# Kernel tuning notes

Hardware: AMD Instinct MI355X
Metric: run time of the kernel (lower is better)

Reference implementation:

```python
import jax, jax.numpy as jnp
import numpy as np

TAU = 0.2  # world.kgc_temp
EPS = 1e-12  # F.normalize eps


def _l2_normalize(z):
    n = jnp.linalg.norm(z, axis=1, keepdims=True)
    return z / jnp.maximum(n, EPS)


def setup_inputs() -> dict:
    key = jax.random.key(0)
    k1, k2 = jax.random.split(key)
    N, D = 8192, 512
    z1 = jax.random.normal(k1, (N, D), dtype=jnp.float32)
    z2 = jax.random.normal(k2, (N, D), dtype=jnp.float32)
    return {"z1": z1, "z2": z2}


def _semi_loss(h1, h2):
    # h1, h2: [N, D] already L2-normalized
    refl_sim = jnp.exp(jnp.matmul(h1, h1.T) / TAU)      # [N, N]
    between_sim = jnp.exp(jnp.matmul(h1, h2.T) / TAU)   # [N, N]
    denom = refl_sim.sum(axis=1) + between_sim.sum(axis=1) - jnp.diag(refl_sim)
    return -jnp.log(jnp.diag(between_sim) / denom)      # [N]


def reference(z1, z2):
    h1 = _l2_normalize(z1)
    h2 = _l2_normalize(z2)
    l1 = _semi_loss(h1, h2)
    l2 = _semi_loss(h2, h1)
    return jnp.sum((l1 + l2) * 0.5)
```

## Files before the change

kernel.cpp:

```cpp
#include <hip/hip_runtime.h>
#include <hip/hip_bf16.h>
#include <math.h>
#include <stdint.h>

#define N_ROWS 8192
#define DIM 512
#define INV_TAU 5.0f
#define EXP5 148.41315910257660342f

typedef float f32x4 __attribute__((ext_vector_type(4)));
typedef long long i64;

union PairU {
  int4 v;
  struct { i64 lo, hi; } s;
};

__device__ __forceinline__ void gload_lds16(const void* g, void* l) {
  __builtin_amdgcn_global_load_lds(
      (__attribute__((address_space(1))) void*)(void*)g,
      (__attribute__((address_space(3))) void*)l,
      16, 0, 0);
}

__global__ __launch_bounds__(256) void normalize_kernel(
    const float* __restrict__ z1, const float* __restrict__ z2,
    uint8_t* __restrict__ h1p, uint8_t* __restrict__ h2p,
    float* __restrict__ dvec,
    float* __restrict__ r1, float* __restrict__ r2,
    float* __restrict__ brow, float* __restrict__ bcol,
    float* __restrict__ out) {
  __shared__ __align__(16) uint8_t L[16384];
  const int t = threadIdx.x;
  const int lr = t >> 4;
  const int kb = t & 15;
  const int row = blockIdx.x * 16 + lr;
  const float4* p1 = (const float4*)(z1 + (size_t)row * DIM + kb * 32);
  const float4* p2 = (const float4*)(z2 + (size_t)row * DIM + kb * 32);
  float4 a[8], b[8];
  float s1 = 0.f, s2 = 0.f, s3 = 0.f;
#pragma unroll
  for (int i = 0; i < 8; i++) {
    a[i] = p1[i]; b[i] = p2[i];
    s1 += a[i].x*a[i].x + a[i].y*a[i].y + a[i].z*a[i].z + a[i].w*a[i].w;
    s2 += b[i].x*b[i].x + b[i].y*b[i].y + b[i].z*b[i].z + b[i].w*b[i].w;
    s3 += a[i].x*b[i].x + a[i].y*b[i].y + a[i].z*b[i].z + a[i].w*b[i].w;
  }
  for (int m = 1; m <= 8; m <<= 1) {
    s1 += __shfl_xor(s1, m);
    s2 += __shfl_xor(s2, m);
    s3 += __shfl_xor(s3, m);
  }
  const float inv1 = 1.0f / fmaxf(sqrtf(s1), 1e-12f);
  const float inv2 = 1.0f / fmaxf(sqrtf(s2), 1e-12f);
  int w1[8], w2[8];
#pragma unroll
  for (int i = 0; i < 8; i++) {
    int w = __builtin_amdgcn_cvt_pk_fp8_f32(a[i].x*inv1, a[i].y*inv1, 0, false);
    w1[i] = __builtin_amdgcn_cvt_pk_fp8_f32(a[i].z*inv1, a[i].w*inv1, w, true);
    w = __builtin_amdgcn_cvt_pk_fp8_f32(b[i].x*inv2, b[i].y*inv2, 0, false);
    w2[i] = __builtin_amdgcn_cvt_pk_fp8_f32(b[i].z*inv2, b[i].w*inv2, w, true);
  }
  union { i64 q; int d[2]; } u;
  const int lbase = (kb >> 1) * 1024 + lr * 16 + (kb & 1) * 8;
#pragma unroll
  for (int q = 0; q < 4; q++) {
    u.d[0] = w1[q*2]; u.d[1] = w1[q*2+1];
    *(i64*)(L + lbase + q * 256) = u.q;
    u.d[0] = w2[q*2]; u.d[1] = w2[q*2+1];
    *(i64*)(L + 8192 + lbase + q * 256) = u.q;
  }
  if (kb == 0) dvec[row] = s3 * inv1 * inv2;
  if (t < 16) {
    const int i = blockIdx.x * 16 + t;
    r1[i] = 0.f; r2[i] = 0.f; brow[i] = 0.f; bcol[i] = 0.f;
    if (i == 0) out[0] = 0.f;
  }
  __syncthreads();
  const size_t gb = (size_t)blockIdx.x * 8192;
  int4* g1 = (int4*)(h1p + gb);
  int4* g2 = (int4*)(h2p + gb);
  const int4* Lv = (const int4*)L;
  g1[t]       = Lv[t];
  g1[t + 256] = Lv[t + 256];
  g2[t]       = Lv[t + 512];
  g2[t + 256] = Lv[t + 768];
}

__global__ __launch_bounds__(512, 4) void expsum_kernel(
    const uint8_t* __restrict__ h1p, const uint8_t* __restrict__ h2p,
    float* __restrict__ r1, float* __restrict__ r2,
    float* __restrict__ brow, float* __restrict__ bcol) {
  __shared__ __align__(16) uint8_t Bs[65536];

  const int u = (blockIdx.x & 7) * 520 + (blockIdx.x >> 3);
  int bi = (int)((129.0 - sqrt(129.0 * 129.0 - 4.0 * (double)u)) * 0.5);
  while (bi * (129 - bi) > u) bi--;
  while ((bi + 1) * (128 - bi) <= u) bi++;
  const int bj = 2 * bi + (u - bi * (129 - bi));
  const bool needPred = (bj == 2 * bi) || (bj == 2 * bi + 1);

  const uint8_t* Ap = (bi < 32) ? h1p : h2p;
  const uint8_t* Bp = (bj < 64) ? h1p : h2p;
  float* rowsOut = (bi < 32) ? ((bj < 64) ? r1 : brow) : r2;
  float* colsOut = (bj < 64) ? r1 : ((bi < 32) ? bcol : r2);
  const int iOutBase = (bi & 31) * 256;
  const int jOutBase = (bj & 63) * 128;
  const int giBase = bi * 256;
  const int gjBase = bj * 128;

  const int t = threadIdx.x;
  const int w = t >> 6;
  const int lane = t & 63;
  const int l16 = lane & 15;
  const int kq = lane >> 4;

  const uint8_t* Abase =
      Ap + ((size_t)((bi & 31) * 16 + w * 2)) * 8192 + (size_t)lane * 16 + 3584;
  const uint8_t* aSt0 = Abase;
  const uint8_t* aSt1 = Abase + 8192;

  PairU Ar[3][2];
#pragma unroll
  for (int p = 0; p < 2; p++) {
    const int ofs = p * 1024 - 3584;
    Ar[p][0].v = *(const int4*)(aSt0 + ofs);
    Ar[p][1].v = *(const int4*)(aSt1 + ofs);
  }

  {
    const uint8_t* Bgp = Bp + (size_t)(bj & 63) * 65536;
#pragma unroll
    for (int rnd = 0; rnd < 8; rnd++)
      gload_lds16(Bgp + rnd * 8192 + t * 16, Bs + rnd * 8192 + t * 16);
  }

  f32x4 acc[2][8];
#pragma unroll
  for (int a = 0; a < 2; a++)
#pragma unroll
    for (int b = 0; b < 8; b++)
#pragma unroll
      for (int r = 0; r < 4; r++) acc[a][b][r] = 0.0f;

  __syncthreads();

#pragma unroll
  for (int kbp = 0; kbp < 8; kbp++) {
    const int cur = kbp % 3;
    if (kbp < 6) {
      const int nxt = (kbp + 2) % 3;
      const int ofs = (kbp + 2) * 1024 - 3584;
      Ar[nxt][0].v = *(const int4*)(aSt0 + ofs);
      Ar[nxt][1].v = *(const int4*)(aSt1 + ofs);
    }
    PairU Bf[8];
#pragma unroll
    for (int f = 0; f < 8; f++)
      Bf[f].v = *(const int4*)(Bs + f * 8192 + kbp * 1024 + lane * 16);
#pragma unroll
    for (int fm = 0; fm < 2; fm++)
#pragma unroll
      for (int fn = 0; fn < 8; fn++)
        acc[fm][fn] = __builtin_amdgcn_mfma_f32_16x16x32_fp8_fp8(
            Ar[cur][fm].s.lo, Bf[fn].s.lo, acc[fm][fn], 0, 0, 0);
#pragma unroll
    for (int fm = 0; fm < 2; fm++)
#pragma unroll
      for (int fn = 0; fn < 8; fn++)
        acc[fm][fn] = __builtin_amdgcn_mfma_f32_16x16x32_fp8_fp8(
            Ar[cur][fm].s.hi, Bf[fn].s.hi, acc[fm][fn], 0, 0, 0);
  }

  float rowp[2][4];
  float colp[8];
#pragma unroll
  for (int fm = 0; fm < 2; fm++)
#pragma unroll
    for (int r = 0; r < 4; r++) rowp[fm][r] = 0.0f;
#pragma unroll
  for (int fn = 0; fn < 8; fn++) colp[fn] = 0.0f;

  if (!needPred) {
#pragma unroll
    for (int fm = 0; fm < 2; fm++)
#pragma unroll
      for (int fn = 0; fn < 8; fn++)
#pragma unroll
        for (int r = 0; r < 4; r++) {
          const float e = __expf(acc[fm][fn][r] * INV_TAU);
          rowp[fm][r] += e;
          colp[fn] += e;
        }
  } else {
#pragma unroll
    for (int fm = 0; fm < 2; fm++)
#pragma unroll
      for (int fn = 0; fn < 8; fn++)
#pragma unroll
        for (int r = 0; r < 4; r++) {
          const int gi = giBase + w * 32 + fm * 16 + kq * 4 + r;
          const int gj = gjBase + fn * 16 + l16;
          const float e = __expf(acc[fm][fn][r] * INV_TAU);
          rowp[fm][r] += (gi <= gj) ? e : 0.0f;
          colp[fn] += (gi < gj) ? e : 0.0f;
        }
  }

  __syncthreads();
  float* lds_col = (float*)Bs;
  float* lds_row = lds_col + 128;
  if (t < 128) lds_col[t] = 0.0f;
  __syncthreads();

#pragma unroll
  for (int fm = 0; fm < 2; fm++) {
#pragma unroll
    for (int r = 0; r < 4; r++) {
      float v = rowp[fm][r];
      v += __shfl_xor(v, 1);
      v += __shfl_xor(v, 2);
      v += __shfl_xor(v, 4);
      v += __shfl_xor(v, 8);
      if (l16 == 0) lds_row[w * 32 + fm * 16 + kq * 4 + r] = v;
    }
  }
#pragma unroll
  for (int fn = 0; fn < 8; fn++) {
    float v = colp[fn];
    v += __shfl_xor(v, 16);
    v += __shfl_xor(v, 32);
    if (kq == 0) atomicAdd(&lds_col[fn * 16 + l16], v);
  }
  __syncthreads();

  if (t < 256) atomicAdd(&rowsOut[iOutBase + t], lds_row[t]);
  else if (t < 384) atomicAdd(&colsOut[jOutBase + (t - 256)], lds_col[t - 256]);
}

__global__ __launch_bounds__(256) void finalize_kernel(
    const float* __restrict__ r1, const float* __restrict__ r2,
    const float* __restrict__ brow, const float* __restrict__ bcol,
    const float* __restrict__ dvec, float* __restrict__ out) {
  const int i = blockIdx.x * 256 + threadIdx.x;
  const float den1 = r1[i] + brow[i] - EXP5;
  const float den2 = r2[i] + bcol[i] - EXP5;
  float v = 0.5f * (logf(den1) + logf(den2)) - INV_TAU * dvec[i];
  for (int m = 32; m; m >>= 1) v += __shfl_xor(v, m);
  __shared__ float red[4];
  const int wave = threadIdx.x >> 6;
  if ((threadIdx.x & 63) == 0) red[wave] = v;
  __syncthreads();
  if (threadIdx.x == 0) atomicAdd(out, red[0] + red[1] + red[2] + red[3]);
}

extern "C" void kernel_launch(void* const* d_in, const int* in_sizes, int n_in,
                              void* d_out, int out_size, void* d_ws, size_t ws_size,
                              hipStream_t stream) {
  const float* z1 = (const float*)d_in[0];
  const float* z2 = (const float*)d_in[1];
  float* out = (float*)d_out;

  char* ws = (char*)d_ws;
  uint8_t* h1p = (uint8_t*)ws;
  uint8_t* h2p = (uint8_t*)(ws + (4u << 20));
  float* r1   = (float*)(ws + (8u << 20));
  float* r2   = r1 + N_ROWS;
  float* brow = r2 + N_ROWS;
  float* bcol = brow + N_ROWS;
  float* dvec = bcol + N_ROWS;

  normalize_kernel<<<N_ROWS / 16, 256, 0, stream>>>(
      z1, z2, h1p, h2p, dvec, r1, r2, brow, bcol, out);
  expsum_kernel<<<4160, 512, 0, stream>>>(h1p, h2p, r1, r2, brow, bcol);
  finalize_kernel<<<N_ROWS / 256, 256, 0, stream>>>(r1, r2, brow, bcol, dvec, out);
}
```

Measured before the change: 207.4 us.

## Switch expsum GEMM to 32x32x16 FP8 MFMA with matching packed layout

The exp-sum kernel now issues 32x32x16 FP8 MFMA instructions with 16-wide accumulators instead of 16x16x32 tiles. Each wave computes a 32x128 tile with fewer, larger MFMAs and fewer LDS B-fragment loads per K step. The normalize kernel is reworked to 32-row blocks of 512 threads so the packed FP8 layout matches the new operand fragments. The epilogue index mapping, the diagonal masking and the row/column reductions are rewritten for the 32x32 output layout. This risks layout or indexing mistakes and changes register pressure.

```diff
diff --git a/kernel.cpp b/kernel.cpp
--- a/kernel.cpp
+++ b/kernel.cpp
@@ -8,7 +8,7 @@
 #define INV_TAU 5.0f
 #define EXP5 148.41315910257660342f
 
-typedef float f32x4 __attribute__((ext_vector_type(4)));
+typedef float f32x16 __attribute__((ext_vector_type(16)));
 typedef long long i64;
 
 union PairU {
@@ -23,18 +23,18 @@
       16, 0, 0);
 }
 
-__global__ __launch_bounds__(256) void normalize_kernel(
+__global__ __launch_bounds__(512) void normalize_kernel(
     const float* __restrict__ z1, const float* __restrict__ z2,
     uint8_t* __restrict__ h1p, uint8_t* __restrict__ h2p,
     float* __restrict__ dvec,
     float* __restrict__ r1, float* __restrict__ r2,
     float* __restrict__ brow, float* __restrict__ bcol,
     float* __restrict__ out) {
-  __shared__ __align__(16) uint8_t L[16384];
+  __shared__ __align__(16) uint8_t L[32768];
   const int t = threadIdx.x;
   const int lr = t >> 4;
   const int kb = t & 15;
-  const int row = blockIdx.x * 16 + lr;
+  const int row = blockIdx.x * 32 + lr;
   const float4* p1 = (const float4*)(z1 + (size_t)row * DIM + kb * 32);
   const float4* p2 = (const float4*)(z2 + (size_t)row * DIM + kb * 32);
   float4 a[8], b[8];
@@ -56,35 +56,30 @@
   int w1[8], w2[8];
 #pragma unroll
   for (int i = 0; i < 8; i++) {
-    int w = __builtin_amdgcn_cvt_pk_fp8_f32(a[i].x*inv1, a[i].y*inv1, 0, false);
-    w1[i] = __builtin_amdgcn_cvt_pk_fp8_f32(a[i].z*inv1, a[i].w*inv1, w, true);
-    w = __builtin_amdgcn_cvt_pk_fp8_f32(b[i].x*inv2, b[i].y*inv2, 0, false);
-    w2[i] = __builtin_amdgcn_cvt_pk_fp8_f32(b[i].z*inv2, b[i].w*inv2, w, true);
-  }
-  union { i64 q; int d[2]; } u;
-  const int lbase = (kb >> 1) * 1024 + lr * 16 + (kb & 1) * 8;
-#pragma unroll
-  for (int q = 0; q < 4; q++) {
-    u.d[0] = w1[q*2]; u.d[1] = w1[q*2+1];
-    *(i64*)(L + lbase + q * 256) = u.q;
-    u.d[0] = w2[q*2]; u.d[1] = w2[q*2+1];
-    *(i64*)(L + 8192 + lbase + q * 256) = u.q;
-  }
+    int wv = __builtin_amdgcn_cvt_pk_fp8_f32(a[i].x*inv1, a[i].y*inv1, 0, false);
+    w1[i] = __builtin_amdgcn_cvt_pk_fp8_f32(a[i].z*inv1, a[i].w*inv1, wv, true);
+    wv = __builtin_amdgcn_cvt_pk_fp8_f32(b[i].x*inv2, b[i].y*inv2, 0, false);
+    w2[i] = __builtin_amdgcn_cvt_pk_fp8_f32(b[i].z*inv2, b[i].w*inv2, wv, true);
+  }
+  *(int4*)(L + kb * 1024 + lr * 16)          = make_int4(w1[0], w1[1], w1[4], w1[5]);
+  *(int4*)(L + kb * 1024 + (lr + 32) * 16)   = make_int4(w1[2], w1[3], w1[6], w1[7]);
+  *(int4*)(L + 16384 + kb * 1024 + lr * 16)        = make_int4(w2[0], w2[1], w2[4], w2[5]);
+  *(int4*)(L + 16384 + kb * 1024 + (lr + 32) * 16) = make_int4(w2[2], w2[3], w2[6], w2[7]);
   if (kb == 0) dvec[row] = s3 * inv1 * inv2;
-  if (t < 16) {
-    const int i = blockIdx.x * 16 + t;
+  if (t < 32) {
+    const int i = blockIdx.x * 32 + t;
     r1[i] = 0.f; r2[i] = 0.f; brow[i] = 0.f; bcol[i] = 0.f;
     if (i == 0) out[0] = 0.f;
   }
   __syncthreads();
-  const size_t gb = (size_t)blockIdx.x * 8192;
+  const size_t gb = (size_t)blockIdx.x * 16384;
   int4* g1 = (int4*)(h1p + gb);
   int4* g2 = (int4*)(h2p + gb);
   const int4* Lv = (const int4*)L;
-  g1[t]       = Lv[t];
-  g1[t + 256] = Lv[t + 256];
-  g2[t]       = Lv[t + 512];
-  g2[t + 256] = Lv[t + 768];
+  g1[t]        = Lv[t];
+  g1[t + 512]  = Lv[t + 512];
+  g2[t]        = Lv[t + 1024];
+  g2[t + 512]  = Lv[t + 1536];
 }
 
 __global__ __launch_bounds__(512, 4) void expsum_kernel(
@@ -112,21 +107,18 @@
   const int t = threadIdx.x;
   const int w = t >> 6;
   const int lane = t & 63;
-  const int l16 = lane & 15;
-  const int kq = lane >> 4;
-
-  const uint8_t* Abase =
-      Ap + ((size_t)((bi & 31) * 16 + w * 2)) * 8192 + (size_t)lane * 16 + 3584;
-  const uint8_t* aSt0 = Abase;
-  const uint8_t* aSt1 = Abase + 8192;
+  const int l32 = lane & 31;
+  const int l5 = lane >> 5;
+
+  const uint8_t* Ag =
+      Ap + ((size_t)((bi & 31) * 8 + w)) * 16384 + (size_t)lane * 16;
+  const uint8_t* aLo = Ag + 4096;
+  const uint8_t* aHi = Ag + 12288;
 
   PairU Ar[3][2];
 #pragma unroll
-  for (int p = 0; p < 2; p++) {
-    const int ofs = p * 1024 - 3584;
-    Ar[p][0].v = *(const int4*)(aSt0 + ofs);
-    Ar[p][1].v = *(const int4*)(aSt1 + ofs);
-  }
+  for (int p = 0; p < 4; p++)
+    Ar[p >> 1][p & 1].v = *(const int4*)(aLo + p * 1024 - 4096);
 
   {
     const uint8_t* Bgp = Bp + (size_t)(bj & 63) * 65536;
@@ -135,13 +127,13 @@
       gload_lds16(Bgp + rnd * 8192 + t * 16, Bs + rnd * 8192 + t * 16);
   }
 
-  f32x4 acc[2][8];
-#pragma unroll
-  for (int a = 0; a < 2; a++)
-#pragma unroll
-    for (int b = 0; b < 8; b++)
-#pragma unroll
-      for (int r = 0; r < 4; r++) acc[a][b][r] = 0.0f;
+  f32x16 acc[4];
+#pragma unroll
+  for (int fn = 0; fn < 4; fn++)
+#pragma unroll
+    for (int r = 0; r < 16; r++) acc[fn][r] = 0.0f;
+
+  const uint8_t* BsL = Bs + lane * 16;
 
   __syncthreads();
 
@@ -150,61 +142,60 @@
     const int cur = kbp % 3;
     if (kbp < 6) {
       const int nxt = (kbp + 2) % 3;
-      const int ofs = (kbp + 2) * 1024 - 3584;
-      Ar[nxt][0].v = *(const int4*)(aSt0 + ofs);
-      Ar[nxt][1].v = *(const int4*)(aSt1 + ofs);
+      const int pp0 = (kbp + 2) * 2;
+#pragma unroll
+      for (int j = 0; j < 2; j++) {
+        const int pp = pp0 + j;
+        Ar[nxt][j].v = (pp < 8)
+            ? *(const int4*)(aLo + pp * 1024 - 4096)
+            : *(const int4*)(aHi + pp * 1024 - 12288);
+      }
     }
-    PairU Bf[8];
-#pragma unroll
-    for (int f = 0; f < 8; f++)
-      Bf[f].v = *(const int4*)(Bs + f * 8192 + kbp * 1024 + lane * 16);
-#pragma unroll
-    for (int fm = 0; fm < 2; fm++)
-#pragma unroll
-      for (int fn = 0; fn < 8; fn++)
-        acc[fm][fn] = __builtin_amdgcn_mfma_f32_16x16x32_fp8_fp8(
-            Ar[cur][fm].s.lo, Bf[fn].s.lo, acc[fm][fn], 0, 0, 0);
-#pragma unroll
-    for (int fm = 0; fm < 2; fm++)
-#pragma unroll
-      for (int fn = 0; fn < 8; fn++)
-        acc[fm][fn] = __builtin_amdgcn_mfma_f32_16x16x32_fp8_fp8(
-            Ar[cur][fm].s.hi, Bf[fn].s.hi, acc[fm][fn], 0, 0, 0);
-  }
-
-  float rowp[2][4];
-  float colp[8];
-#pragma unroll
-  for (int fm = 0; fm < 2; fm++)
-#pragma unroll
-    for (int r = 0; r < 4; r++) rowp[fm][r] = 0.0f;
-#pragma unroll
-  for (int fn = 0; fn < 8; fn++) colp[fn] = 0.0f;
+#pragma unroll
+    for (int j = 0; j < 2; j++) {
+      const int pp = kbp * 2 + j;
+      PairU Bf[4];
+#pragma unroll
+      for (int fn = 0; fn < 4; fn++)
+        Bf[fn].v = *(const int4*)(BsL + fn * 16384 + pp * 1024);
+#pragma unroll
+      for (int fn = 0; fn < 4; fn++)
+        acc[fn] = __builtin_amdgcn_mfma_f32_32x32x16_fp8_fp8(
+            Ar[cur][j].s.lo, Bf[fn].s.lo, acc[fn], 0, 0, 0);
+#pragma unroll
+      for (int fn = 0; fn < 4; fn++)
+        acc[fn] = __builtin_amdgcn_mfma_f32_32x32x16_fp8_fp8(
+            Ar[cur][j].s.hi, Bf[fn].s.hi, acc[fn], 0, 0, 0);
+    }
+  }
+
+  float rowp[16];
+  float colp[4];
+#pragma unroll
+  for (int r = 0; r < 16; r++) rowp[r] = 0.0f;
+#pragma unroll
+  for (int fn = 0; fn < 4; fn++) colp[fn] = 0.0f;
 
   if (!needPred) {
 #pragma unroll
-    for (int fm = 0; fm < 2; fm++)
-#pragma unroll
-      for (int fn = 0; fn < 8; fn++)
-#pragma unroll
-        for (int r = 0; r < 4; r++) {
-          const float e = __expf(acc[fm][fn][r] * INV_TAU);
-          rowp[fm][r] += e;
-          colp[fn] += e;
-        }
+    for (int fn = 0; fn < 4; fn++)
+#pragma unroll
+      for (int r = 0; r < 16; r++) {
+        const float e = __expf(acc[fn][r] * INV_TAU);
+        rowp[r] += e;
+        colp[fn] += e;
+      }
   } else {
 #pragma unroll
-    for (int fm = 0; fm < 2; fm++)
-#pragma unroll
-      for (int fn = 0; fn < 8; fn++)
-#pragma unroll
-        for (int r = 0; r < 4; r++) {
-          const int gi = giBase + w * 32 + fm * 16 + kq * 4 + r;
-          const int gj = gjBase + fn * 16 + l16;
-          const float e = __expf(acc[fm][fn][r] * INV_TAU);
-          rowp[fm][r] += (gi <= gj) ? e : 0.0f;
-          colp[fn] += (gi < gj) ? e : 0.0f;
-        }
+    for (int fn = 0; fn < 4; fn++)
+#pragma unroll
+      for (int r = 0; r < 16; r++) {
+        const int gi = giBase + w * 32 + 4 * l5 + (r & 3) + 8 * (r >> 2);
+        const int gj = gjBase + fn * 32 + l32;
+        const float e = __expf(acc[fn][r] * INV_TAU);
+        rowp[r] += (gi <= gj) ? e : 0.0f;
+        colp[fn] += (gi < gj) ? e : 0.0f;
+      }
   }
 
   __syncthreads();
@@ -214,23 +205,20 @@
   __syncthreads();
 
 #pragma unroll
-  for (int fm = 0; fm < 2; fm++) {
-#pragma unroll
-    for (int r = 0; r < 4; r++) {
-      float v = rowp[fm][r];
-      v += __shfl_xor(v, 1);
-      v += __shfl_xor(v, 2);
-      v += __shfl_xor(v, 4);
-      v += __shfl_xor(v, 8);
-      if (l16 == 0) lds_row[w * 32 + fm * 16 + kq * 4 + r] = v;
-    }
-  }
-#pragma unroll
-  for (int fn = 0; fn < 8; fn++) {
+  for (int r = 0; r < 16; r++) {
+    float v = rowp[r];
+    v += __shfl_xor(v, 1);
+    v += __shfl_xor(v, 2);
+    v += __shfl_xor(v, 4);
+    v += __shfl_xor(v, 8);
+    v += __shfl_xor(v, 16);
+    if (l32 == 0) lds_row[w * 32 + 4 * l5 + (r & 3) + 8 * (r >> 2)] = v;
+  }
+#pragma unroll
+  for (int fn = 0; fn < 4; fn++) {
     float v = colp[fn];
-    v += __shfl_xor(v, 16);
     v += __shfl_xor(v, 32);
-    if (kq == 0) atomicAdd(&lds_col[fn * 16 + l16], v);
+    if (l5 == 0) atomicAdd(&lds_col[fn * 32 + l32], v);
   }
   __syncthreads();
 
@@ -270,7 +258,7 @@
   float* bcol = brow + N_ROWS;
   float* dvec = bcol + N_ROWS;
 
-  normalize_kernel<<<N_ROWS / 16, 256, 0, stream>>>(
+  normalize_kernel<<<N_ROWS / 32, 512, 0, stream>>>(
       z1, z2, h1p, h2p, dvec, r1, r2, brow, bcol, out);
   expsum_kernel<<<4160, 512, 0, stream>>>(h1p, h2p, r1, r2, brow, bcol);
   finalize_kernel<<<N_ROWS / 256, 256, 0, stream>>>(r1, r2, brow, bcol, dvec, out);
```

New measurement: 210.7 us. Within noise of the previous version (+1.6%).
